# Kernel tuning notes

Measured on AMD Instinct MI355X. Metric: run time of the kernel, lower is better.

## Reference

```python
import jax, jax.numpy as jnp
import numpy as np

N, K, C_IN, C_OUT, KNN_DIM = 16384, 16, 64, 64, 8
LN_EPS = 1e-5


def _layer_norm(h, g, b):
    m = jnp.mean(h, axis=-1, keepdims=True)
    v = jnp.mean(jnp.square(h - m), axis=-1, keepdims=True)
    return (h - m) * jax.lax.rsqrt(v + LN_EPS) * g + b


def setup_inputs() -> dict:
    key = jax.random.key(0)
    ks = jax.random.split(key, 10)

    def lin(k, fan_out, fan_in):
        bound = 1.0 / np.sqrt(fan_in)
        kw, kb = jax.random.split(k)
        W = jax.random.uniform(kw, (fan_out, fan_in), jnp.float32, -bound, bound)
        b = jax.random.uniform(kb, (fan_out,), jnp.float32, -bound, bound)
        return W, b

    Ws, bs = lin(ks[4], KNN_DIM, C_IN)
    W1, b1 = lin(ks[5], C_OUT, 2 * C_IN)
    W2, b2 = lin(ks[6], C_OUT, C_OUT)
    return {
        "x": jax.random.normal(ks[0], (N, C_IN), jnp.float32),
        "edge_index": jax.random.randint(ks[1], (2, N * K), 0, N, jnp.int64),
        "eta": jax.random.normal(ks[2], (N,), jnp.float32),
        "phi": jax.random.normal(ks[3], (N,), jnp.float32),
        "Ws": Ws, "bs": bs,
        "W1": W1, "b1": b1,
        "g1": jnp.ones((C_OUT,), jnp.float32), "be1": jnp.zeros((C_OUT,), jnp.float32),
        "W2": W2, "b2": b2,
        "g2": jnp.ones((C_OUT,), jnp.float32), "be2": jnp.zeros((C_OUT,), jnp.float32),
    }


def reference(x, edge_index, eta, phi, Ws, bs, W1, b1, g1, be1, W2, b2, g2, be2):
    # edge_index/eta/phi are accepted but unused, as in the torch module:
    # the kNN graph is rebuilt dynamically in the lin_s-projected space.
    s = x @ Ws.T + bs                                  # [N, KNN_DIM]
    sq = jnp.sum(s * s, axis=-1)                       # [N]
    d2 = sq[:, None] + sq[None, :] - 2.0 * (s @ s.T)   # [N, N] squared L2
    _, idx = jax.lax.top_k(-d2, K)                     # [N, K] neighbor (source) ids

    x_j = x[idx]                                       # [N, K, C_IN] gather sources
    x_i = jnp.broadcast_to(x[:, None, :], x_j.shape)   # [N, K, C_IN] target feats
    feat = jnp.concatenate([x_i, x_j - x_i], axis=-1)  # [N, K, 2*C_IN]

    h = jax.nn.relu(_layer_norm(feat @ W1.T + b1, g1, be1))
    h = jax.nn.relu(_layer_norm(h @ W2.T + b2, g2, be2))
    return jnp.mean(h, axis=1)                         # mean aggregation over K edges
```

## Files before the change

### kernel.cpp

```cpp
#include <hip/hip_runtime.h>

#define N_PTS 16384
#define KNN   16
#define CIN   64
#define SDIM  8

typedef __bf16 bf16x8 __attribute__((ext_vector_type(8)));
typedef float  f32x4  __attribute__((ext_vector_type(4)));

__global__ __launch_bounds__(64) void k_proj(
    const float* __restrict__ x, const float* __restrict__ Ws, const float* __restrict__ bs,
    __bf16* __restrict__ qvec, __bf16* __restrict__ cvec, double* __restrict__ s64) {
  __shared__ double w[SDIM * CIN];
  __shared__ double bsh[SDIM];
  int tid = threadIdx.x;
  for (int t = tid; t < SDIM * CIN; t += 64) w[t] = (double)Ws[t];
  if (tid < SDIM) bsh[tid] = (double)bs[tid];
  __syncthreads();
  int i = blockIdx.x * 64 + tid;
  double acc[SDIM];
#pragma unroll
  for (int d = 0; d < SDIM; ++d) acc[d] = bsh[d];
  for (int j = 0; j < CIN; j += 4) {
    float4 xv = *(const float4*)(x + (size_t)i * CIN + j);
#pragma unroll
    for (int d = 0; d < SDIM; ++d) {
      acc[d] = fma((double)xv.x, w[d * CIN + j + 0], acc[d]);
      acc[d] = fma((double)xv.y, w[d * CIN + j + 1], acc[d]);
      acc[d] = fma((double)xv.z, w[d * CIN + j + 2], acc[d]);
      acc[d] = fma((double)xv.w, w[d * CIN + j + 3], acc[d]);
    }
  }
  float sf[8];
  float sq = 0.f;
#pragma unroll
  for (int d = 0; d < SDIM; ++d) {
    sf[d] = (float)acc[d];
    s64[(size_t)i * SDIM + d] = acc[d];
    sq = fmaf(sf[d], sf[d], sq);
  }
  __bf16 av[32], bv[32];
#pragma unroll
  for (int d = 0; d < 8; ++d) {
    __bf16 hi = (__bf16)sf[d];
    float hif = (float)hi;
    __bf16 lo = (__bf16)(sf[d] - hif);
    av[d] = hi; av[8 + d] = hi; av[16 + d] = lo;
    __bf16 h2 = (__bf16)(-2.f * hif);
    __bf16 l2 = (__bf16)(-2.f * (float)lo);
    bv[d] = h2; bv[8 + d] = l2; bv[16 + d] = h2;
  }
  __bf16 sqh = (__bf16)sq;
  __bf16 sql = (__bf16)(sq - (float)sqh);
  __bf16 one = (__bf16)1.0f, zero = (__bf16)0.0f;
  __bf16 eps = (__bf16)0.0009765625f;
  av[24] = sqh; av[25] = sql; av[26] = one; av[27] = one;
  av[28] = one; av[29] = av[30] = av[31] = zero;
  bv[24] = one; bv[25] = one; bv[26] = sqh; bv[27] = sql;
  bv[28] = eps; bv[29] = bv[30] = bv[31] = zero;
  uint4* ap = (uint4*)av;
  uint4* bpv = (uint4*)bv;
  uint4* da = (uint4*)(qvec + (size_t)i * 32);
  uint4* db = (uint4*)(cvec + (size_t)i * 32);
  da[0] = ap[0]; da[1] = ap[1]; da[2] = ap[2]; da[3] = ap[3];
  db[0] = bpv[0]; db[1] = bpv[1]; db[2] = bpv[2]; db[3] = bpv[3];
}

__device__ inline unsigned bitonic64(unsigned key, int lane) {
#pragma unroll
  for (int size = 2; size <= 64; size <<= 1) {
#pragma unroll
    for (int stride = size >> 1; stride > 0; stride >>= 1) {
      unsigned other = __shfl_xor(key, stride, 64);
      bool takeMin = (((lane & size) == 0) == ((lane & stride) == 0));
      unsigned mn = min(key, other), mx = max(key, other);
      key = takeMin ? mn : mx;
    }
  }
  return key;
}

__global__ __launch_bounds__(256) void k_dist(
    const __bf16* __restrict__ qvec, const __bf16* __restrict__ cvec,
    unsigned* __restrict__ partial) {
  __shared__ unsigned ring[32 * 256];
  const int tid = threadIdx.x;
  const int lane = tid & 63;
  const int wv = tid >> 6;
  const int e = lane & 15, g = lane >> 4;
  const int qidx = blockIdx.x * 64 + wv * 16 + e;
  const int cbase = blockIdx.y * 4096;

  bf16x8 Qf = *(const bf16x8*)(qvec + (size_t)qidx * 32 + g * 8);

  unsigned kk[16];
#pragma unroll
  for (int r = 0; r < 16; ++r) kk[r] = 0xFFFFFFFFu;
  float thr = __uint_as_float(0x7F800000u);
  unsigned cnt = 0;

  const __bf16* cp = cvec + (size_t)(cbase + e) * 32 + g * 8;
  f32x4 zero4 = (f32x4){0.f, 0.f, 0.f, 0.f};
  const unsigned cb0 = (unsigned)(cbase + 4 * g);

  auto consume4 = [&](const f32x4& v, unsigned cb) {
#pragma unroll
    for (int j = 0; j < 4; ++j) {
      unsigned key = (__float_as_uint(v[j]) & 0xFFFFC000u) | (cb + j);
      ring[(cnt << 8) | (unsigned)tid] = key;
      cnt += (v[j] < thr) ? 1u : 0u;
    }
  };
  auto storm = [&]() {
#pragma unroll 1
    for (int i = 0; i < 32; ++i) {
      if (!__any(i < (int)cnt)) break;
      unsigned key = ring[(i << 8) | (unsigned)tid];
      if (i >= (int)cnt) key = 0xFFFFFFFFu;
      if (__any(key < kk[15])) {
#pragma unroll
        for (int r = 15; r > 0; --r) kk[r] = max(kk[r - 1], min(kk[r], key));
        kk[0] = min(kk[0], key);
      }
    }
    cnt = 0;
    unsigned tbk = min((kk[15] >> 14) + 1u, 0x1FE00u);
    thr = __uint_as_float(tbk << 14);
    thr = fminf(thr, __shfl_xor(thr, 16, 64));
    thr = fminf(thr, __shfl_xor(thr, 32, 64));
  };

#define LOADG(B, grp) { const __bf16* np_ = cp + (size_t)(grp) * 2048;           \
    B##0 = *(const bf16x8*)(np_);        B##1 = *(const bf16x8*)(np_ + 512);     \
    B##2 = *(const bf16x8*)(np_ + 1024); B##3 = *(const bf16x8*)(np_ + 1536); }
#define MFMAG(C, B) {                                                            \
    C##0 = __builtin_amdgcn_mfma_f32_16x16x32_bf16(B##0, Qf, zero4, 0, 0, 0);    \
    C##1 = __builtin_amdgcn_mfma_f32_16x16x32_bf16(B##1, Qf, zero4, 0, 0, 0);    \
    C##2 = __builtin_amdgcn_mfma_f32_16x16x32_bf16(B##2, Qf, zero4, 0, 0, 0);    \
    C##3 = __builtin_amdgcn_mfma_f32_16x16x32_bf16(B##3, Qf, zero4, 0, 0, 0); }
#define CONSG(C, grp) { unsigned cb_ = cb0 + (unsigned)(grp) * 64u;              \
    consume4(C##0, cb_); consume4(C##1, cb_ + 16); consume4(C##2, cb_ + 32);     \
    consume4(C##3, cb_ + 48);                                                    \
    if (__any(cnt >= 17)) storm(); }

  bf16x8 a00, a01, a02, a03, a10, a11, a12, a13;
  f32x4 c00, c01, c02, c03, c10, c11, c12, c13;

  LOADG(a0, 0)
  LOADG(a1, 1)
  MFMAG(c0, a0)
  for (int gr = 0; gr < 62; gr += 2) {
    LOADG(a0, gr + 2)
    MFMAG(c1, a1)
    CONSG(c0, gr)
    LOADG(a1, gr + 3)
    MFMAG(c0, a0)
    CONSG(c1, gr + 1)
  }
  MFMAG(c1, a1)
  CONSG(c0, 62)
  CONSG(c1, 63)
  storm();
#undef LOADG
#undef MFMAG
#undef CONSG

  unsigned* p = partial + (size_t)qidx * 256 + (size_t)blockIdx.y * 64 + g * 16;
  *(uint4*)(p + 0)  = make_uint4(kk[0], kk[1], kk[2], kk[3]);
  *(uint4*)(p + 4)  = make_uint4(kk[4], kk[5], kk[6], kk[7]);
  *(uint4*)(p + 8)  = make_uint4(kk[8], kk[9], kk[10], kk[11]);
  *(uint4*)(p + 12) = make_uint4(kk[12], kk[13], kk[14], kk[15]);
}

__global__ __launch_bounds__(256) void k_merge(
    const double* __restrict__ s64, const unsigned* __restrict__ partial,
    unsigned short* __restrict__ fin) {
  int lane = threadIdx.x & 63;
  int node = blockIdx.x * 4 + (threadIdx.x >> 6);
  unsigned jc = 0;
#pragma unroll
  for (int t = 0; t < 4; ++t) {
    unsigned key = partial[(size_t)node * 256 + t * 64 + lane];
    key = bitonic64(key, lane);
    unsigned k16 = __shfl(key, lane & 15, 64);
    if ((lane >> 4) == t) jc = k16 & 0x3FFFu;
  }
  const double* si = s64 + (size_t)node * 8;
  const double* sj = s64 + (size_t)jc * 8;
  double d2 = 0.0;
#pragma unroll
  for (int d = 0; d < 8; ++d) { double t = si[d] - sj[d]; d2 = fma(t, t, d2); }
  unsigned long long key =
      (((unsigned long long)__double_as_longlong(d2)) & ~0x3FFFull) | (unsigned long long)jc;
#pragma unroll
  for (int size = 2; size <= 64; size <<= 1) {
#pragma unroll
    for (int stride = size >> 1; stride > 0; stride >>= 1) {
      unsigned lo = __shfl_xor((unsigned)key, stride, 64);
      unsigned hi = __shfl_xor((unsigned)(key >> 32), stride, 64);
      unsigned long long other = ((unsigned long long)hi << 32) | lo;
      bool takeMin = (((lane & size) == 0) == ((lane & stride) == 0));
      unsigned long long mn = key < other ? key : other;
      unsigned long long mx = key < other ? other : key;
      key = takeMin ? mn : mx;
    }
  }
  if (lane < 16) fin[(size_t)node * 16 + lane] = (unsigned short)(key & 0x3FFFull);
}

__device__ inline bf16x8 pack8(float4 a, float4 b) {
  bf16x8 r;
  r[0] = (__bf16)a.x; r[1] = (__bf16)a.y; r[2] = (__bf16)a.z; r[3] = (__bf16)a.w;
  r[4] = (__bf16)b.x; r[5] = (__bf16)b.y; r[6] = (__bf16)b.z; r[7] = (__bf16)b.w;
  return r;
}
__device__ inline float4 sub4(float4 a, float4 b) {
  return make_float4(a.x - b.x, a.y - b.y, a.z - b.z, a.w - b.w);
}
__device__ inline void ln_relu(const f32x4 acc[4], const float bc[4], const float gc[4],
                               const float bec[4], float nh[4][4]) {
#pragma unroll
  for (int j = 0; j < 4; ++j) {
    float v0 = acc[0][j] + bc[0], v1 = acc[1][j] + bc[1];
    float v2 = acc[2][j] + bc[2], v3 = acc[3][j] + bc[3];
    float t = v0 + v1 + v2 + v3;
    float qq = v0 * v0 + v1 * v1 + v2 * v2 + v3 * v3;
#pragma unroll
    for (int m = 1; m < 16; m <<= 1) {
      t += __shfl_xor(t, m, 64);
      qq += __shfl_xor(qq, m, 64);
    }
    float mean = t * (1.f / 64.f);
    float var = qq * (1.f / 64.f) - mean * mean;
    float rstd = rsqrtf(var + 1e-5f);
    nh[0][j] = fmaxf((v0 - mean) * rstd * gc[0] + bec[0], 0.f);
    nh[1][j] = fmaxf((v1 - mean) * rstd * gc[1] + bec[1], 0.f);
    nh[2][j] = fmaxf((v2 - mean) * rstd * gc[2] + bec[2], 0.f);
    nh[3][j] = fmaxf((v3 - mean) * rstd * gc[3] + bec[3], 0.f);
  }
}

__global__ __launch_bounds__(256) void k_mlp(
    const float* __restrict__ x, const unsigned short* __restrict__ nbr,
    const float* __restrict__ W1, const float* __restrict__ b1,
    const float* __restrict__ g1v, const float* __restrict__ be1,
    const float* __restrict__ W2, const float* __restrict__ b2,
    const float* __restrict__ g2v, const float* __restrict__ be2,
    float* __restrict__ out) {
  __shared__ float tr[4][16 * 68];
  const int lane = threadIdx.x & 63;
  const int wv = threadIdx.x >> 6;
  const int e = lane & 15;
  const int g = lane >> 4;

  bf16x8 B1[4][4];
#pragma unroll
  for (int ks = 0; ks < 4; ++ks)
#pragma unroll
    for (int nt = 0; nt < 4; ++nt) {
      const float* wr = W1 + (size_t)(nt * 16 + e) * 128 + ks * 32 + g * 8;
#pragma unroll
      for (int u = 0; u < 8; ++u) B1[ks][nt][u] = (__bf16)wr[u];
    }
  bf16x8 B2[2][4];
#pragma unroll
  for (int ks = 0; ks < 2; ++ks)
#pragma unroll
    for (int nt = 0; nt < 4; ++nt) {
      const float* wr = W2 + (size_t)(nt * 16 + e) * 64 + ks * 32 + g * 8;
#pragma unroll
      for (int u = 0; u < 8; ++u) B2[ks][nt][u] = (__bf16)wr[u];
    }
  float b1c[4], g1c[4], be1c[4], b2c[4], g2c[4], be2c[4];
#pragma unroll
  for (int nt = 0; nt < 4; ++nt) {
    int c = nt * 16 + e;
    b1c[nt] = b1[c]; g1c[nt] = g1v[c]; be1c[nt] = be1[c];
    b2c[nt] = b2[c]; g2c[nt] = g2v[c]; be2c[nt] = be2[c];
  }

  for (int it = 0; it < 8; ++it) {
    int node = (blockIdx.x * 4 + wv) * 8 + it;
    int jidx = nbr[(size_t)node * 16 + e];
    const float* xi = x + (size_t)node * 64;
    const float* xj = x + (size_t)jidx * 64;
    float4 xi0a = *(const float4*)(xi + g * 8),      xi0b = *(const float4*)(xi + g * 8 + 4);
    float4 xi1a = *(const float4*)(xi + 32 + g * 8), xi1b = *(const float4*)(xi + 32 + g * 8 + 4);
    float4 xj0a = *(const float4*)(xj + g * 8),      xj0b = *(const float4*)(xj + g * 8 + 4);
    float4 xj1a = *(const float4*)(xj + 32 + g * 8), xj1b = *(const float4*)(xj + 32 + g * 8 + 4);
    bf16x8 Af[4];
    Af[0] = pack8(xi0a, xi0b);
    Af[1] = pack8(xi1a, xi1b);
    Af[2] = pack8(sub4(xj0a, xi0a), sub4(xj0b, xi0b));
    Af[3] = pack8(sub4(xj1a, xi1a), sub4(xj1b, xi1b));

    f32x4 acc[4];
#pragma unroll
    for (int nt = 0; nt < 4; ++nt) acc[nt] = (f32x4){0.f, 0.f, 0.f, 0.f};
#pragma unroll
    for (int ks = 0; ks < 4; ++ks)
#pragma unroll
      for (int nt = 0; nt < 4; ++nt)
        acc[nt] = __builtin_amdgcn_mfma_f32_16x16x32_bf16(Af[ks], B1[ks][nt], acc[nt], 0, 0, 0);

    float nh[4][4];
    ln_relu(acc, b1c, g1c, be1c, nh);

    float* T = tr[wv];
#pragma unroll
    for (int nt = 0; nt < 4; ++nt)
#pragma unroll
      for (int j = 0; j < 4; ++j) T[(4 * g + j) * 68 + nt * 16 + e] = nh[nt][j];
    bf16x8 A2[2];
#pragma unroll
    for (int ks = 0; ks < 2; ++ks) {
      float4 ha = *(const float4*)(T + e * 68 + ks * 32 + g * 8);
      float4 hb = *(const float4*)(T + e * 68 + ks * 32 + g * 8 + 4);
      A2[ks] = pack8(ha, hb);
    }

    f32x4 acc2[4];
#pragma unroll
    for (int nt = 0; nt < 4; ++nt) acc2[nt] = (f32x4){0.f, 0.f, 0.f, 0.f};
#pragma unroll
    for (int ks = 0; ks < 2; ++ks)
#pragma unroll
      for (int nt = 0; nt < 4; ++nt)
        acc2[nt] = __builtin_amdgcn_mfma_f32_16x16x32_bf16(A2[ks], B2[ks][nt], acc2[nt], 0, 0, 0);

    float nh2[4][4];
    ln_relu(acc2, b2c, g2c, be2c, nh2);

#pragma unroll
    for (int nt = 0; nt < 4; ++nt) {
      float p = nh2[nt][0] + nh2[nt][1] + nh2[nt][2] + nh2[nt][3];
      p += __shfl_xor(p, 16, 64);
      p += __shfl_xor(p, 32, 64);
      if (g == 0) out[(size_t)node * 64 + nt * 16 + e] = p * 0.0625f;
    }
  }
}

extern "C" void kernel_launch(void* const* d_in, const int* in_sizes, int n_in,
                              void* d_out, int out_size, void* d_ws, size_t ws_size,
                              hipStream_t stream) {
  (void)in_sizes; (void)n_in; (void)out_size; (void)ws_size;
  const float* x   = (const float*)d_in[0];
  const float* Ws  = (const float*)d_in[4];
  const float* bs  = (const float*)d_in[5];
  const float* W1  = (const float*)d_in[6];
  const float* b1  = (const float*)d_in[7];
  const float* g1  = (const float*)d_in[8];
  const float* be1 = (const float*)d_in[9];
  const float* W2  = (const float*)d_in[10];
  const float* b2  = (const float*)d_in[11];
  const float* g2  = (const float*)d_in[12];
  const float* be2 = (const float*)d_in[13];
  float* out = (float*)d_out;

  char* ws = (char*)d_ws;
  __bf16* qvec = (__bf16*)(ws);
  __bf16* cvec = (__bf16*)(ws + 1048576);
  double* s64  = (double*)(ws + 2097152);
  unsigned* partial   = (unsigned*)(ws + 3145728);
  unsigned short* fin = (unsigned short*)(ws + 19922944);

  k_proj<<<dim3(256), dim3(64), 0, stream>>>(x, Ws, bs, qvec, cvec, s64);
  k_dist<<<dim3(256, 4), dim3(256), 0, stream>>>(qvec, cvec, partial);
  k_merge<<<dim3(4096), dim3(256), 0, stream>>>(s64, partial, fin);
  k_mlp<<<dim3(512), dim3(256), 0, stream>>>(x, fin, W1, b1, g1, be1, W2, b2, g2, be2, out);
}
```

Before: 183.9 us.

## Seed kNN threshold from a probe tile and skip candidate groups above it

Adds a small pre-pass kernel that runs one MFMA tile per query against 16 far-away candidates and stores the worst distance as an upper-bound threshold. The distance kernel starts from this seeded threshold rather than infinity, and skips writing whole 4-value MFMA outputs to the LDS ring when no lane has a value below the threshold. Fewer ring writes and storm merges are expected, at the cost of an extra kernel launch. Merge now forces unfilled (sentinel) entries to infinite distance, since partial lists may no longer contain 16 real candidates.

```diff
diff --git a/kernel.cpp b/kernel.cpp
--- a/kernel.cpp
+++ b/kernel.cpp
@@ -66,6 +66,26 @@
   db[0] = bpv[0]; db[1] = bpv[1]; db[2] = bpv[2]; db[3] = bpv[3];
 }
 
+__global__ __launch_bounds__(256) void k_seed(
+    const __bf16* __restrict__ qvec, const __bf16* __restrict__ cvec,
+    float* __restrict__ thr0v) {
+  const int lane = threadIdx.x & 63;
+  const int wv = threadIdx.x >> 6;
+  const int e = lane & 15, g = lane >> 4;
+  const int qt = blockIdx.x * 4 + wv;
+  const int qidx = qt * 16 + e;
+  const int pr = (qt * 16 + 8192) & 16383;
+  bf16x8 Qf = *(const bf16x8*)(qvec + (size_t)qidx * 32 + g * 8);
+  bf16x8 Af = *(const bf16x8*)(cvec + (size_t)(pr + e) * 32 + g * 8);
+  f32x4 z = (f32x4){0.f, 0.f, 0.f, 0.f};
+  f32x4 v = __builtin_amdgcn_mfma_f32_16x16x32_bf16(Af, Qf, z, 0, 0, 0);
+  float m = fmaxf(fmaxf(v[0], v[1]), fmaxf(v[2], v[3]));
+  m = fmaxf(m, __shfl_xor(m, 16, 64));
+  m = fmaxf(m, __shfl_xor(m, 32, 64));
+  unsigned tb = min((__float_as_uint(m) >> 14) + 1u, 0x1FE00u);
+  if (g == 0) thr0v[qidx] = __uint_as_float(tb << 14);
+}
+
 __device__ inline unsigned bitonic64(unsigned key, int lane) {
 #pragma unroll
   for (int size = 2; size <= 64; size <<= 1) {
@@ -82,7 +102,7 @@
 
 __global__ __launch_bounds__(256) void k_dist(
     const __bf16* __restrict__ qvec, const __bf16* __restrict__ cvec,
-    unsigned* __restrict__ partial) {
+    const float* __restrict__ thr0v, unsigned* __restrict__ partial) {
   __shared__ unsigned ring[32 * 256];
   const int tid = threadIdx.x;
   const int lane = tid & 63;
@@ -96,7 +116,7 @@
   unsigned kk[16];
 #pragma unroll
   for (int r = 0; r < 16; ++r) kk[r] = 0xFFFFFFFFu;
-  float thr = __uint_as_float(0x7F800000u);
+  float thr = thr0v[qidx];
   unsigned cnt = 0;
 
   const __bf16* cp = cvec + (size_t)(cbase + e) * 32 + g * 8;
@@ -125,9 +145,10 @@
     }
     cnt = 0;
     unsigned tbk = min((kk[15] >> 14) + 1u, 0x1FE00u);
-    thr = __uint_as_float(tbk << 14);
-    thr = fminf(thr, __shfl_xor(thr, 16, 64));
-    thr = fminf(thr, __shfl_xor(thr, 32, 64));
+    float nthr = __uint_as_float(tbk << 14);
+    nthr = fminf(nthr, __shfl_xor(nthr, 16, 64));
+    nthr = fminf(nthr, __shfl_xor(nthr, 32, 64));
+    thr = fminf(thr, nthr);
   };
 
 #define LOADG(B, grp) { const __bf16* np_ = cp + (size_t)(grp) * 2048;           \
@@ -138,9 +159,12 @@
     C##1 = __builtin_amdgcn_mfma_f32_16x16x32_bf16(B##1, Qf, zero4, 0, 0, 0);    \
     C##2 = __builtin_amdgcn_mfma_f32_16x16x32_bf16(B##2, Qf, zero4, 0, 0, 0);    \
     C##3 = __builtin_amdgcn_mfma_f32_16x16x32_bf16(B##3, Qf, zero4, 0, 0, 0); }
+#define CONS1(Cv, cbv) {                                                         \
+    float m4_ = fminf(fminf(Cv[0], Cv[1]), fminf(Cv[2], Cv[3]));                 \
+    if (__any(m4_ < thr)) consume4(Cv, cbv); }
 #define CONSG(C, grp) { unsigned cb_ = cb0 + (unsigned)(grp) * 64u;              \
-    consume4(C##0, cb_); consume4(C##1, cb_ + 16); consume4(C##2, cb_ + 32);     \
-    consume4(C##3, cb_ + 48);                                                    \
+    CONS1(C##0, cb_) CONS1(C##1, cb_ + 16) CONS1(C##2, cb_ + 32)                 \
+    CONS1(C##3, cb_ + 48)                                                        \
     if (__any(cnt >= 17)) storm(); }
 
   bf16x8 a00, a01, a02, a03, a10, a11, a12, a13;
@@ -163,6 +187,7 @@
   storm();
 #undef LOADG
 #undef MFMAG
+#undef CONS1
 #undef CONSG
 
   unsigned* p = partial + (size_t)qidx * 256 + (size_t)blockIdx.y * 64 + g * 16;
@@ -178,18 +203,20 @@
   int lane = threadIdx.x & 63;
   int node = blockIdx.x * 4 + (threadIdx.x >> 6);
   unsigned jc = 0;
+  unsigned kc = 0xFFFFFFFFu;
 #pragma unroll
   for (int t = 0; t < 4; ++t) {
     unsigned key = partial[(size_t)node * 256 + t * 64 + lane];
     key = bitonic64(key, lane);
     unsigned k16 = __shfl(key, lane & 15, 64);
-    if ((lane >> 4) == t) jc = k16 & 0x3FFFu;
+    if ((lane >> 4) == t) { jc = k16 & 0x3FFFu; kc = k16; }
   }
   const double* si = s64 + (size_t)node * 8;
   const double* sj = s64 + (size_t)jc * 8;
   double d2 = 0.0;
 #pragma unroll
   for (int d = 0; d < 8; ++d) { double t = si[d] - sj[d]; d2 = fma(t, t, d2); }
+  if (kc >= 0x80000000u) d2 = (double)INFINITY;
   unsigned long long key =
       (((unsigned long long)__double_as_longlong(d2)) & ~0x3FFFull) | (unsigned long long)jc;
 #pragma unroll
@@ -364,9 +391,11 @@
   double* s64  = (double*)(ws + 2097152);
   unsigned* partial   = (unsigned*)(ws + 3145728);
   unsigned short* fin = (unsigned short*)(ws + 19922944);
+  float* thr0v = (float*)(ws + 20447232);
 
   k_proj<<<dim3(256), dim3(64), 0, stream>>>(x, Ws, bs, qvec, cvec, s64);
-  k_dist<<<dim3(256, 4), dim3(256), 0, stream>>>(qvec, cvec, partial);
+  k_seed<<<dim3(256), dim3(256), 0, stream>>>(qvec, cvec, thr0v);
+  k_dist<<<dim3(256, 4), dim3(256), 0, stream>>>(qvec, cvec, thr0v, partial);
   k_merge<<<dim3(4096), dim3(256), 0, stream>>>(s64, partial, fin);
   k_mlp<<<dim3(512), dim3(256), 0, stream>>>(x, fin, W1, b1, g1, be1, W2, b2, g2, be2, out);
 }
```

Measured after the change: 195.5 us. +6.3%, slower.
